# Kernel optimization log

Hardware: AMD Instinct MI355X
Metric: run time of the kernel (lower is better)

Reference implementation:

```python
import jax, jax.numpy as jnp
import numpy as np
from jax import lax

M_POINT = 1024
NSAMPLE = 16
GRASPNESS_THRESHOLD = 0.1
HMIN, HMAX = -0.02, 0.04  # cylinder height range (GraspNet CloudCrop)
RADII = (0.025, 0.05, 0.075, 0.1)
BIG = 1e10


def _fps(xyz, mask):
    """Masked furthest point sampling. xyz [N,3], mask [N] bool -> idx [M_POINT] int32.
    Masked-out points carry -BIG min-distance so they are never selected."""
    first = jnp.argmax(mask).astype(jnp.int32)  # first graspable point (ragged FPS start)
    dists = jnp.where(mask, BIG, -BIG)
    idxs = jnp.zeros((M_POINT,), jnp.int32).at[0].set(first)

    def body(i, carry):
        idxs, dists = carry
        last = xyz[idxs[i - 1]]
        d = jnp.sum((xyz - last) ** 2, axis=-1)
        dists = jnp.where(mask, jnp.minimum(dists, d), -BIG)
        nxt = jnp.argmax(dists).astype(jnp.int32)
        return idxs.at[i].set(nxt), dists

    idxs, _ = lax.fori_loop(1, M_POINT, body, (idxs, dists))
    return idxs


def _cylinder_crop(xyz_g, feat_g, rot, radius, w1, b1, w2, b2):
    """Cylinder query + group + shared MLP + maxpool.
    xyz_g [B,M,3], feat_g [B,M,C], rot [B,M,3,3] -> [B,M,256]."""
    B, M, _ = xyz_g.shape
    # offsets of candidate n relative to seed m, expressed in the seed's gripper frame
    diff = xyz_g[:, None, :, :] - xyz_g[:, :, None, :]          # [B,M(seed),M(cand),3]
    local = jnp.einsum('bmnj,bmji->bmni', diff, rot)            # rotate into approach frame
    along = local[..., 0]
    r2 = local[..., 1] ** 2 + local[..., 2] ** 2
    cond = (r2 < radius * radius) & (along > HMIN) & (along < HMAX)  # [B,M,M]
    # first NSAMPLE in-cylinder indices (ball-query semantics: pad with first hit)
    order = jnp.where(cond, jnp.arange(M)[None, None, :], M)
    sel = jnp.argsort(order, axis=-1)[..., :NSAMPLE].astype(jnp.int32)  # [B,M,NS]
    cnt = cond.sum(axis=-1)                                     # [B,M]
    fill = sel[..., :1]
    idx = jnp.where(jnp.arange(NSAMPLE)[None, None, :] < cnt[..., None], sel, fill)
    idx = jnp.where(cnt[..., None] > 0, idx, 0)
    grouped_xyz = jnp.take_along_axis(local, idx[..., None], axis=2) / radius  # [B,M,NS,3]
    grouped_feat = feat_g[jnp.arange(B)[:, None, None], idx]                    # [B,M,NS,C]
    g = jnp.concatenate([grouped_xyz, grouped_feat], axis=-1)                   # [B,M,NS,3+C]
    h = jax.nn.relu(jnp.einsum('bmnf,of->bmno', g, w1) + b1)
    h = jax.nn.relu(jnp.einsum('bmnf,of->bmno', h, w2) + b2)
    return h.max(axis=2)                                                        # [B,M,256]


def setup_inputs() -> dict:
    key = jax.random.key(0)
    ks = jax.random.split(key, 10)
    B, N, C = 4, 20000, 512
    return {
        'seed_xyz': jax.random.normal(ks[0], (B, N, 3), jnp.float32),
        'seed_features': jax.random.normal(ks[1], (B, C, N), jnp.float32),
        'objectness_score': jax.random.normal(ks[2], (B, 2, N), jnp.float32),
        'graspness_score': jax.random.uniform(ks[3], (B, N), jnp.float32),
        'grasp_top_views_rot': jax.random.normal(ks[4], (B, M_POINT, 3, 3), jnp.float32),
        'crop_w1': jax.random.normal(ks[5], (4, 256, 3 + C), jnp.float32) * 0.05,
        'crop_b1': jnp.zeros((4, 256), jnp.float32),
        'crop_w2': jax.random.normal(ks[6], (4, 256, 256), jnp.float32) * 0.05,
        'crop_b2': jnp.zeros((4, 256), jnp.float32),
        'fuse_w': jax.random.normal(ks[7], (256, 1024), jnp.float32) * 0.05,
        'fuse_b': jnp.zeros((256,), jnp.float32),
    }


def reference(seed_xyz, seed_features, objectness_score, graspness_score,
              grasp_top_views_rot, crop_w1, crop_b1, crop_w2, crop_b2,
              fuse_w, fuse_b):
    # graspable mask (per-point, data dependent)
    objectness_mask = jnp.argmax(objectness_score, axis=1) == 1       # [B,N]
    graspness_mask = graspness_score > GRASPNESS_THRESHOLD
    graspable_mask = objectness_mask & graspness_mask
    # masked FPS per sample, then gather
    idxs = jax.vmap(_fps)(seed_xyz, graspable_mask)                    # [B,M]
    xyz_g = jnp.take_along_axis(seed_xyz, idxs[:, :, None], axis=1)    # [B,M,3]
    feat = seed_features.transpose(0, 2, 1)                            # [B,N,C]
    feat_g = jnp.take_along_axis(feat, idxs[:, :, None], axis=1)       # [B,M,C]
    # multiscale cylinder crops
    feats = [_cylinder_crop(xyz_g, feat_g, grasp_top_views_rot, RADII[k],
                            crop_w1[k], crop_b1[k], crop_w2[k], crop_b2[k])
             for k in range(4)]
    cat = jnp.concatenate(feats, axis=-1)                              # [B,M,1024]
    fused = jnp.einsum('bmf,of->bom', cat, fuse_w) + fuse_b[None, :, None]  # [B,256,M]
    return fused
```

## Files before the change

kernel.cpp:

```cpp
#include <hip/hip_runtime.h>
#include <cstdint>
#include <cfloat>
#include <climits>

#define NPTS 20000
#define NB 4
#define MP 1024
#define CF 512
#define MAXCH 20
#define PFIX 10
#define KFAST (PFIX*MP)

__constant__ float c_r2[4]  = { (float)(0.025*0.025), (float)(0.05*0.05),
                                (float)(0.075*0.075), (float)(0.1*0.1) };
__constant__ float c_rad[4] = { 0.025f, 0.05f, 0.075f, 0.1f };

__global__ __launch_bounds__(1024, 4)
void k_fps(const float* __restrict__ xyz, const float* __restrict__ obj,
           const float* __restrict__ grasp, int* __restrict__ idxs,
           float* __restrict__ xyz_g,
           float* __restrict__ xc, float* __restrict__ yc,
           float* __restrict__ zc, int* __restrict__ ci)
{
    const int b = blockIdx.x;
    const int tid = threadIdx.x;
    const int lane = tid & 63, wid = tid >> 6;
    const float* xb  = xyz   + (size_t)b * NPTS * 3;
    const float* ob0 = obj   + (size_t)b * 2 * NPTS;
    const float* ob1 = ob0 + NPTS;
    const float* gb  = grasp + (size_t)b * NPTS;
    float* xcb = xc + (size_t)b * 20480;
    float* ycb = yc + (size_t)b * 20480;
    float* zcb = zc + (size_t)b * 20480;
    int*   cib = ci + (size_t)b * 20480;

    __shared__ float sXYZ[3 * KFAST];
    __shared__ int   s_sel[MP];
    __shared__ unsigned long long sKey[2][16];
    __shared__ int   sWaveCnt[16];
    float* sX = sXYZ;
    float* sY = sXYZ + KFAST;
    float* sZ = sXYZ + 2 * KFAST;

    int kbase = 0;
    for (int i = 0; i < MAXCH; ++i) {
        int n = i * MP + tid;
        bool msk = false; float x = 0.f, y = 0.f, z = 0.f;
        if (n < NPTS) {
            msk = (ob1[n] > ob0[n]) && (gb[n] > 0.1f);
            if (msk) { x = xb[n*3+0]; y = xb[n*3+1]; z = xb[n*3+2]; }
        }
        unsigned long long bal = __ballot(msk);
        if (lane == 0) sWaveCnt[wid] = __popcll(bal);
        __syncthreads();
        int pre = 0, tot = 0;
        for (int w = 0; w < 16; ++w) { int c = sWaveCnt[w]; tot += c; if (w < wid) pre += c; }
        if (msk) {
            int rank = kbase + pre + __popcll(bal & ((1ull << lane) - 1ull));
            xcb[rank] = x; ycb[rank] = y; zcb[rank] = z; cib[rank] = n;
            if (rank < KFAST) { sX[rank] = x; sY[rank] = y; sZ[rank] = z; }
        }
        kbase += tot;
        __syncthreads();
    }
    const int K = kbase;

    if (K == 0) {
        idxs[b*MP + tid] = 0;
        xyz_g[((size_t)b*MP + tid)*3 + 0] = xb[0];
        xyz_g[((size_t)b*MP + tid)*3 + 1] = xb[1];
        xyz_g[((size_t)b*MP + tid)*3 + 2] = xb[2];
        return;
    }

    if (K <= KFAST) {
        float px[PFIX], py[PFIX], pz[PFIX], pd[PFIX];
#pragma unroll
        for (int i = 0; i < PFIX; ++i) {
            int c = tid + (i << 10);
            bool v = c < K;
            px[i] = v ? sX[c] : 0.f;
            py[i] = v ? sY[c] : 0.f;
            pz[i] = v ? sZ[c] : 0.f;
            pd[i] = v ? 1e10f : -3.0e38f;
        }
        float lx = sX[0], ly = sY[0], lz = sZ[0];
        if (tid == 0) s_sel[0] = 0;

        for (int it = 1; it < MP; ++it) {
            float bv = -3.4e38f; int bn = 0;
#pragma unroll
            for (int i = 0; i < PFIX; ++i) {
                float dx = px[i] - lx, dy = py[i] - ly, dz = pz[i] - lz;
                float d = __fadd_rn(__fadd_rn(__fmul_rn(dx,dx), __fmul_rn(dy,dy)),
                                    __fmul_rn(dz,dz));
                float nd = fminf(pd[i], d);
                pd[i] = nd;
                bool w = nd > bv;
                bn = w ? (tid + (i << 10)) : bn;
                bv = fmaxf(bv, nd);
            }
            unsigned int ob = __float_as_uint(bv);
            unsigned int ord = (ob & 0x80000000u) ? ~ob : (ob | 0x80000000u);
            unsigned long long key = ((unsigned long long)ord << 32)
                                   | (unsigned int)(~bn);
#pragma unroll
            for (int off = 1; off < 64; off <<= 1) {
                unsigned long long ok = __shfl_xor(key, off);
                key = (ok > key) ? ok : key;
            }
            int p = it & 1;
            if (lane == 0) sKey[p][wid] = key;
            __syncthreads();
            unsigned long long k2 = sKey[p][lane & 15];
#pragma unroll
            for (int off = 1; off < 16; off <<= 1) {
                unsigned long long ok = __shfl_xor(k2, off);
                k2 = (ok > k2) ? ok : k2;
            }
            int n = ~((unsigned int)k2);
            lx = sX[n]; ly = sY[n]; lz = sZ[n];
            if (tid == 0) s_sel[it] = n;
        }
        __syncthreads();
        int nc = s_sel[tid];
        idxs[b*MP + tid] = cib[nc];
        xyz_g[((size_t)b*MP + tid)*3 + 0] = sX[nc];
        xyz_g[((size_t)b*MP + tid)*3 + 1] = sY[nc];
        xyz_g[((size_t)b*MP + tid)*3 + 2] = sZ[nc];
        return;
    }

    {
        float* fD = sXYZ;
        for (int c = tid; c < K; c += MP) fD[c] = 1e10f;
        float lx = xcb[0], ly = ycb[0], lz = zcb[0];
        if (tid == 0) s_sel[0] = 0;
        __syncthreads();
        for (int it = 1; it < MP; ++it) {
            float bv = -3.4e38f; int bn = 0;
            for (int c = tid; c < K; c += MP) {
                float dx = xcb[c] - lx, dy = ycb[c] - ly, dz = zcb[c] - lz;
                float d = __fadd_rn(__fadd_rn(__fmul_rn(dx,dx), __fmul_rn(dy,dy)),
                                    __fmul_rn(dz,dz));
                float nd = fminf(fD[c], d);
                fD[c] = nd;
                bool w = nd > bv;
                bn = w ? c : bn;
                bv = fmaxf(bv, nd);
            }
            unsigned int ob = __float_as_uint(bv);
            unsigned int ord = (ob & 0x80000000u) ? ~ob : (ob | 0x80000000u);
            unsigned long long key = ((unsigned long long)ord << 32)
                                   | (unsigned int)(~bn);
#pragma unroll
            for (int off = 1; off < 64; off <<= 1) {
                unsigned long long ok = __shfl_xor(key, off);
                key = (ok > key) ? ok : key;
            }
            int p = it & 1;
            if (lane == 0) sKey[p][wid] = key;
            __syncthreads();
            unsigned long long k2 = sKey[p][lane & 15];
#pragma unroll
            for (int off = 1; off < 16; off <<= 1) {
                unsigned long long ok = __shfl_xor(k2, off);
                k2 = (ok > k2) ? ok : k2;
            }
            int n = ~((unsigned int)k2);
            lx = xcb[n]; ly = ycb[n]; lz = zcb[n];
            if (tid == 0) s_sel[it] = n;
        }
        __syncthreads();
        int nc = s_sel[tid];
        idxs[b*MP + tid] = cib[nc];
        xyz_g[((size_t)b*MP + tid)*3 + 0] = xcb[nc];
        xyz_g[((size_t)b*MP + tid)*3 + 1] = ycb[nc];
        xyz_g[((size_t)b*MP + tid)*3 + 2] = zcb[nc];
    }
}

__global__ void k_gather_feat(const float* __restrict__ sf, const int* __restrict__ idxs,
                              float* __restrict__ feat_g)
{
    int bm = blockIdx.x;
    int b = bm >> 10;
    int n = idxs[bm];
    const float* src = sf + (size_t)b*CF*NPTS + n;
    float* dst = feat_g + (size_t)bm*CF;
    for (int c = threadIdx.x; c < CF; c += 256) dst[c] = src[(size_t)c * NPTS];
}

__global__ void k_prep(const float* __restrict__ w1, const float* __restrict__ w2,
                       float* __restrict__ w2t, float* __restrict__ w1x)
{
    int k = blockIdx.x, cb = blockIdx.y*32, ob = blockIdx.z*32;
    int tx = threadIdx.x & 31, ty = threadIdx.x >> 5;
    __shared__ float t[32][33];
    for (int r = ty; r < 32; r += 8)
        t[r][tx] = w2[((size_t)k*256 + ob + r)*256 + cb + tx];
    __syncthreads();
    for (int r = ty; r < 32; r += 8)
        w2t[((size_t)k*256 + cb + r)*256 + ob + tx] = t[tx][r];
    if (blockIdx.y == 0 && blockIdx.z == 0) {
        int o = threadIdx.x;
        for (int d = 0; d < 3; ++d)
            w1x[(k*3 + d)*256 + o] = w1[((size_t)k*256 + o)*515 + d];
    }
}

__global__ __launch_bounds__(256)
void k_f1(const float* __restrict__ feat_g, const float* __restrict__ w1,
          const float* __restrict__ b1, float* __restrict__ F1)
{
    const int rt = blockIdx.x * 64;
    const int ot = blockIdx.y * 64;
    const int k  = blockIdx.z;
    const int tid = threadIdx.x;
    __shared__ float As[16][68];
    __shared__ float Bs[16][68];
    const int lr = tid >> 2;
    const int lc = (tid & 3) * 4;
    const int tr = (tid & 15) * 4;
    const int tc = (tid >> 4) * 4;
    float acc[4][4] = {};
    for (int kk = 0; kk < CF; kk += 16) {
        const float* ap = feat_g + (size_t)(rt + lr)*CF + kk + lc;
        As[lc+0][lr] = ap[0]; As[lc+1][lr] = ap[1];
        As[lc+2][lr] = ap[2]; As[lc+3][lr] = ap[3];
        const float* bp = w1 + (size_t)(k*256 + ot + lr)*515 + 3 + kk + lc;
        Bs[lc+0][lr] = bp[0]; Bs[lc+1][lr] = bp[1];
        Bs[lc+2][lr] = bp[2]; Bs[lc+3][lr] = bp[3];
        __syncthreads();
#pragma unroll
        for (int cc = 0; cc < 16; ++cc) {
            float a0=As[cc][tr+0], a1=As[cc][tr+1], a2=As[cc][tr+2], a3=As[cc][tr+3];
            float q0=Bs[cc][tc+0], q1=Bs[cc][tc+1], q2=Bs[cc][tc+2], q3=Bs[cc][tc+3];
            acc[0][0]+=a0*q0; acc[0][1]+=a0*q1; acc[0][2]+=a0*q2; acc[0][3]+=a0*q3;
            acc[1][0]+=a1*q0; acc[1][1]+=a1*q1; acc[1][2]+=a1*q2; acc[1][3]+=a1*q3;
            acc[2][0]+=a2*q0; acc[2][1]+=a2*q1; acc[2][2]+=a2*q2; acc[2][3]+=a2*q3;
            acc[3][0]+=a3*q0; acc[3][1]+=a3*q1; acc[3][2]+=a3*q2; acc[3][3]+=a3*q3;
        }
        __syncthreads();
    }
#pragma unroll
    for (int i = 0; i < 4; ++i)
#pragma unroll
        for (int j = 0; j < 4; ++j)
            F1[((size_t)k*4096 + rt+tr+i)*256 + ot+tc+j] = acc[i][j] + b1[k*256 + ot+tc+j];
}

__global__ __launch_bounds__(1024)
void k_nbr(const float* __restrict__ xyz_g, const float* __restrict__ rot,
           int* __restrict__ sel, float* __restrict__ lxyz, int* __restrict__ cnt)
{
    const int bm = blockIdx.x;
    const int b = bm >> 10;
    const int tid = threadIdx.x;
    const int lane = tid & 63, wid = tid >> 6;
    __shared__ float sR[9], sC[3];
    __shared__ int   sSel[4][16];
    __shared__ float sL[4][16][3];
    __shared__ int   sW[16];
    __shared__ int   sCnt[4];
    __shared__ float sFb[3];
    if (tid < 9) sR[tid] = rot[(size_t)bm*9 + tid];
    if (tid < 3) sC[tid] = xyz_g[(size_t)bm*3 + tid];
    __syncthreads();
    float x = xyz_g[((size_t)b*MP + tid)*3 + 0];
    float y = xyz_g[((size_t)b*MP + tid)*3 + 1];
    float z = xyz_g[((size_t)b*MP + tid)*3 + 2];
    float dx = x - sC[0], dy = y - sC[1], dz = z - sC[2];
    float l0 = __fadd_rn(__fadd_rn(__fmul_rn(dx,sR[0]), __fmul_rn(dy,sR[3])), __fmul_rn(dz,sR[6]));
    float l1 = __fadd_rn(__fadd_rn(__fmul_rn(dx,sR[1]), __fmul_rn(dy,sR[4])), __fmul_rn(dz,sR[7]));
    float l2 = __fadd_rn(__fadd_rn(__fmul_rn(dx,sR[2]), __fmul_rn(dy,sR[5])), __fmul_rn(dz,sR[8]));
    float r2 = __fadd_rn(__fmul_rn(l1,l1), __fmul_rn(l2,l2));
    bool basec = (l0 > -0.02f) && (l0 < 0.04f);
    if (tid == 0) { sFb[0]=l0; sFb[1]=l1; sFb[2]=l2; }
    for (int k = 0; k < 4; ++k) {
        bool c = basec && (r2 < c_r2[k]);
        unsigned long long bal = __ballot(c);
        if (lane == 0) sW[wid] = __popcll(bal);
        __syncthreads();
        int pre = 0, tot = 0;
        for (int w = 0; w < 16; ++w) { int cw = sW[w]; tot += cw; if (w < wid) pre += cw; }
        int rank = pre + __popcll(bal & ((1ull << lane) - 1ull));
        if (c && rank < 16) {
            sSel[k][rank] = tid;
            sL[k][rank][0] = l0; sL[k][rank][1] = l1; sL[k][rank][2] = l2;
        }
        if (tid == 0) sCnt[k] = min(tot, 16);
        __syncthreads();
    }
    if (tid < 64) {
        int k = tid >> 4, j = tid & 15;
        int ck = sCnt[k];
        int src = (j < ck) ? j : 0;
        int v; float a0, a1, a2;
        if (ck > 0) { v = sSel[k][src]; a0=sL[k][src][0]; a1=sL[k][src][1]; a2=sL[k][src][2]; }
        else        { v = 0; a0=sFb[0]; a1=sFb[1]; a2=sFb[2]; }
        size_t off = ((size_t)bm*4 + k)*16 + j;
        sel[off] = v;
        lxyz[off*3+0]=a0; lxyz[off*3+1]=a1; lxyz[off*3+2]=a2;
        if (j == 0) cnt[bm*4 + k] = (ck > 0) ? ck : 1;
    }
}

__global__ __launch_bounds__(256)
void k_mlp(const float* __restrict__ F1, const float* __restrict__ w1x,
           const float* __restrict__ w2t, const float* __restrict__ b2,
           const int* __restrict__ sel, const float* __restrict__ lxyz,
           const int* __restrict__ cnt, float* __restrict__ cat)
{
    const int gid = blockIdx.x;
    const int k = gid & 3;
    const int g0 = (gid >> 2) * 4;
    const int o = threadIdx.x;
    __shared__ float h1s[64][256];
    int u0 = cnt[(g0+0)*4 + k], u1 = cnt[(g0+1)*4 + k],
        u2 = cnt[(g0+2)*4 + k], u3 = cnt[(g0+3)*4 + k];
    int off1 = u0, off2 = u0+u1, off3 = off2+u2, tot = off3+u3;
    const float wx0 = w1x[(k*3+0)*256 + o];
    const float wx1 = w1x[(k*3+1)*256 + o];
    const float wx2 = w1x[(k*3+2)*256 + o];
    const float rad = c_rad[k];
    const int bbase = (g0 >> 10) * MP;
    for (int r = 0; r < tot; ++r) {
        int t = (r >= off1) + (r >= off2) + (r >= off3);
        int toff = (t==0) ? 0 : ((t==1) ? off1 : ((t==2) ? off2 : off3));
        int j = r - toff;
        int bmk = (g0 + t)*4 + k;
        int n = sel[(size_t)bmk*16 + j];
        float lx = lxyz[((size_t)bmk*16 + j)*3 + 0];
        float ly = lxyz[((size_t)bmk*16 + j)*3 + 1];
        float lz = lxyz[((size_t)bmk*16 + j)*3 + 2];
        float v = F1[((size_t)k*4096 + bbase + n)*256 + o];
        v += (lx/rad)*wx0 + (ly/rad)*wx1 + (lz/rad)*wx2;
        h1s[r][o] = fmaxf(v, 0.f);
    }
    __syncthreads();
    const float b2v = b2[k*256 + o];
    float m0=0.f, m1=0.f, m2=0.f, m3=0.f;
    const float* w2c = w2t + (size_t)k*65536 + o;
    for (int base = 0; base < tot; base += 4) {
        int r0 = base;
        int r1 = min(base+1, tot-1);
        int r2 = min(base+2, tot-1);
        int r3 = min(base+3, tot-1);
        float a0=0.f, a1=0.f, a2=0.f, a3=0.f;
        for (int c = 0; c < 256; c += 4) {
            float wA = w2c[(c+0)*256], wB = w2c[(c+1)*256];
            float wC = w2c[(c+2)*256], wD = w2c[(c+3)*256];
            float4 h;
            h = *(const float4*)&h1s[r0][c]; a0 += h.x*wA + h.y*wB + h.z*wC + h.w*wD;
            h = *(const float4*)&h1s[r1][c]; a1 += h.x*wA + h.y*wB + h.z*wC + h.w*wD;
            h = *(const float4*)&h1s[r2][c]; a2 += h.x*wA + h.y*wB + h.z*wC + h.w*wD;
            h = *(const float4*)&h1s[r3][c]; a3 += h.x*wA + h.y*wB + h.z*wC + h.w*wD;
        }
#pragma unroll
        for (int q = 0; q < 4; ++q) {
            int r = base + q;
            if (r < tot) {
                float a = (q==0) ? a0 : ((q==1) ? a1 : ((q==2) ? a2 : a3));
                int t = (r >= off1) + (r >= off2) + (r >= off3);
                float val = fmaxf(a + b2v, 0.f);
                if      (t==0) m0 = fmaxf(m0, val);
                else if (t==1) m1 = fmaxf(m1, val);
                else if (t==2) m2 = fmaxf(m2, val);
                else           m3 = fmaxf(m3, val);
            }
        }
    }
    cat[(size_t)(g0+0)*1024 + k*256 + o] = m0;
    cat[(size_t)(g0+1)*1024 + k*256 + o] = m1;
    cat[(size_t)(g0+2)*1024 + k*256 + o] = m2;
    cat[(size_t)(g0+3)*1024 + k*256 + o] = m3;
}

__global__ void k_transpose(const float* __restrict__ cat, float* __restrict__ catT)
{
    int bt = blockIdx.x;
    int b = bt >> 10;
    int t2 = bt & 1023;
    int mi = (t2 >> 5) * 32, fi = (t2 & 31) * 32;
    int tx = threadIdx.x & 31, ty = threadIdx.x >> 5;
    __shared__ float t[32][33];
    const float* src = cat + (size_t)b * 1048576;
    float* dst = catT + (size_t)b * 1048576;
    for (int r = ty; r < 32; r += 8) t[r][tx] = src[(size_t)(mi + r)*1024 + fi + tx];
    __syncthreads();
    for (int r = ty; r < 32; r += 8) dst[(size_t)(fi + r)*1024 + mi + tx] = t[tx][r];
}

__global__ __launch_bounds__(256)
void k_fuse(const float* __restrict__ catT, const float* __restrict__ fw,
            const float* __restrict__ fb, float* __restrict__ out)
{
    const int o0 = blockIdx.x * 4;
    const int b = blockIdx.y;
    const int m = threadIdx.x * 4;
    const float* ct = catT + (size_t)b * 1048576 + m;
    float4 a0 = {0,0,0,0}, a1 = a0, a2 = a0, a3 = a0;
    for (int f = 0; f < 1024; ++f) {
        const float4 cv = *(const float4*)(ct + (size_t)f*1024);
        float w0 = fw[(size_t)(o0+0)*1024 + f];
        float w1 = fw[(size_t)(o0+1)*1024 + f];
        float w2 = fw[(size_t)(o0+2)*1024 + f];
        float w3 = fw[(size_t)(o0+3)*1024 + f];
        a0.x += cv.x*w0; a0.y += cv.y*w0; a0.z += cv.z*w0; a0.w += cv.w*w0;
        a1.x += cv.x*w1; a1.y += cv.y*w1; a1.z += cv.z*w1; a1.w += cv.w*w1;
        a2.x += cv.x*w2; a2.y += cv.y*w2; a2.z += cv.z*w2; a2.w += cv.w*w2;
        a3.x += cv.x*w3; a3.y += cv.y*w3; a3.z += cv.z*w3; a3.w += cv.w*w3;
    }
#pragma unroll
    for (int q = 0; q < 4; ++q) {
        float bb = fb[o0+q];
        float4 r = (q==0) ? a0 : ((q==1) ? a1 : ((q==2) ? a2 : a3));
        r.x += bb; r.y += bb; r.z += bb; r.w += bb;
        *(float4*)&out[((size_t)b*256 + o0 + q)*1024 + m] = r;
    }
}

extern "C" void kernel_launch(void* const* d_in, const int* in_sizes, int n_in,
                              void* d_out, int out_size, void* d_ws, size_t ws_size,
                              hipStream_t stream)
{
    const float* seed_xyz      = (const float*)d_in[0];
    const float* seed_features = (const float*)d_in[1];
    const float* objectness    = (const float*)d_in[2];
    const float* graspness     = (const float*)d_in[3];
    const float* rot           = (const float*)d_in[4];
    const float* w1            = (const float*)d_in[5];
    const float* b1            = (const float*)d_in[6];
    const float* w2            = (const float*)d_in[7];
    const float* b2            = (const float*)d_in[8];
    const float* fw            = (const float*)d_in[9];
    const float* fb            = (const float*)d_in[10];
    float* out = (float*)d_out;

    char* ws = (char*)d_ws;
    size_t off = 0;
    int*   idxs   = (int*)(ws + off);  off += 16u<<10;
    float* xyz_g  = (float*)(ws + off); off += 48u<<10;
    float* feat_g = (float*)(ws + off); off += 8u<<20;
    float* F1     = (float*)(ws + off); off += 16u<<20;
    float* w2t    = (float*)(ws + off); off += 1u<<20;
    float* w1x    = (float*)(ws + off); off += 64u<<10;
    int*   sel    = (int*)(ws + off);   off += 1u<<20;
    int*   cnt    = (int*)(ws + off);   off += 64u<<10;
    float* lxyz   = (float*)(ws + off); off += 3u<<20;
    float* cat    = (float*)(ws + off); off += 16u<<20;
    float* catT   = (float*)(ws + off); off += 16u<<20;

    float* xc = cat;
    float* yc = cat + 4*20480;
    float* zc = cat + 8*20480;
    int*   ci = (int*)(cat + 12*20480);

    k_fps<<<NB, 1024, 0, stream>>>(seed_xyz, objectness, graspness, idxs, xyz_g,
                                   xc, yc, zc, ci);
    k_prep<<<dim3(4,8,8), 256, 0, stream>>>(w1, w2, w2t, w1x);
    k_gather_feat<<<NB*MP, 256, 0, stream>>>(seed_features, idxs, feat_g);
    k_f1<<<dim3(64,4,4), 256, 0, stream>>>(feat_g, w1, b1, F1);
    k_nbr<<<NB*MP, 1024, 0, stream>>>(xyz_g, rot, sel, lxyz, cnt);
    k_mlp<<<4096, 256, 0, stream>>>(F1, w1x, w2t, b2, sel, lxyz, cnt, cat);
    k_transpose<<<4096, 256, 0, stream>>>(cat, catT);
    k_fuse<<<dim3(64,4), 256, 0, stream>>>(catT, fw, fb, out);
}
```

Before: 2.047 ms.

## Use 8 working wavefronts and DPP-based key reductions in fast FPS path

```diff
diff --git a/kernel.cpp b/kernel.cpp
--- a/kernel.cpp
+++ b/kernel.cpp
@@ -9,11 +9,31 @@
 #define CF 512
 #define MAXCH 20
 #define PFIX 10
-#define KFAST (PFIX*MP)
+#define KFAST 10240
+#define NWORK 8
+#define PPT 20
 
 __constant__ float c_r2[4]  = { (float)(0.025*0.025), (float)(0.05*0.05),
                                 (float)(0.075*0.075), (float)(0.1*0.1) };
 __constant__ float c_rad[4] = { 0.025f, 0.05f, 0.075f, 0.1f };
+
+#define DPP_XOR1   0xB1
+#define DPP_XOR2   0x4E
+#define DPP_HMIRR  0x141
+#define DPP_MIRR   0x140
+#define DPP_BC15   0x142
+#define DPP_BC31   0x143
+
+template<int CTRL>
+__device__ __forceinline__ unsigned long long kmax_step(unsigned long long k)
+{
+    unsigned int lo = (unsigned int)k;
+    unsigned int hi = (unsigned int)(k >> 32);
+    unsigned int olo = (unsigned int)__builtin_amdgcn_update_dpp((int)lo, (int)lo, CTRL, 0xf, 0xf, false);
+    unsigned int ohi = (unsigned int)__builtin_amdgcn_update_dpp((int)hi, (int)hi, CTRL, 0xf, 0xf, false);
+    unsigned long long ok = ((unsigned long long)ohi << 32) | (unsigned long long)olo;
+    return (ok > k) ? ok : k;
+}
 
 __global__ __launch_bounds__(1024, 4)
 void k_fps(const float* __restrict__ xyz, const float* __restrict__ obj,
@@ -74,53 +94,59 @@
     }
 
     if (K <= KFAST) {
-        float px[PFIX], py[PFIX], pz[PFIX], pd[PFIX];
-#pragma unroll
-        for (int i = 0; i < PFIX; ++i) {
-            int c = tid + (i << 10);
-            bool v = c < K;
-            px[i] = v ? sX[c] : 0.f;
-            py[i] = v ? sY[c] : 0.f;
-            pz[i] = v ? sZ[c] : 0.f;
-            pd[i] = v ? 1e10f : -3.0e38f;
+        const bool work = (wid < NWORK);
+        float px[PPT], py[PPT], pz[PPT], pd[PPT];
+        if (work) {
+#pragma unroll
+            for (int i = 0; i < PPT; ++i) {
+                int c = tid + (i << 9);
+                bool v = c < K;
+                px[i] = v ? sX[c] : 0.f;
+                py[i] = v ? sY[c] : 0.f;
+                pz[i] = v ? sZ[c] : 0.f;
+                pd[i] = v ? 1e10f : -3.0e38f;
+            }
         }
         float lx = sX[0], ly = sY[0], lz = sZ[0];
         if (tid == 0) s_sel[0] = 0;
 
         for (int it = 1; it < MP; ++it) {
-            float bv = -3.4e38f; int bn = 0;
-#pragma unroll
-            for (int i = 0; i < PFIX; ++i) {
-                float dx = px[i] - lx, dy = py[i] - ly, dz = pz[i] - lz;
-                float d = __fadd_rn(__fadd_rn(__fmul_rn(dx,dx), __fmul_rn(dy,dy)),
-                                    __fmul_rn(dz,dz));
-                float nd = fminf(pd[i], d);
-                pd[i] = nd;
-                bool w = nd > bv;
-                bn = w ? (tid + (i << 10)) : bn;
-                bv = fmaxf(bv, nd);
-            }
-            unsigned int ob = __float_as_uint(bv);
-            unsigned int ord = (ob & 0x80000000u) ? ~ob : (ob | 0x80000000u);
-            unsigned long long key = ((unsigned long long)ord << 32)
-                                   | (unsigned int)(~bn);
-#pragma unroll
-            for (int off = 1; off < 64; off <<= 1) {
-                unsigned long long ok = __shfl_xor(key, off);
-                key = (ok > key) ? ok : key;
-            }
-            int p = it & 1;
-            if (lane == 0) sKey[p][wid] = key;
+            const int p = it & 1;
+            if (work) {
+                float bv = -3.4e38f; int bn = 0;
+#pragma unroll
+                for (int i = 0; i < PPT; ++i) {
+                    float dx = px[i] - lx, dy = py[i] - ly, dz = pz[i] - lz;
+                    float d = __fadd_rn(__fadd_rn(__fmul_rn(dx,dx), __fmul_rn(dy,dy)),
+                                        __fmul_rn(dz,dz));
+                    float nd = fminf(pd[i], d);
+                    pd[i] = nd;
+                    bool w = nd > bv;
+                    bn = w ? (tid + (i << 9)) : bn;
+                    bv = fmaxf(bv, nd);
+                }
+                unsigned int ob = __float_as_uint(bv);
+                unsigned int ord = (ob & 0x80000000u) ? ~ob : (ob | 0x80000000u);
+                unsigned long long key = ((unsigned long long)ord << 32)
+                                       | (unsigned int)(~bn);
+                key = kmax_step<DPP_XOR1 >(key);
+                key = kmax_step<DPP_XOR2 >(key);
+                key = kmax_step<DPP_HMIRR>(key);
+                key = kmax_step<DPP_MIRR >(key);
+                key = kmax_step<DPP_BC15 >(key);
+                key = kmax_step<DPP_BC31 >(key);
+                if (lane == 63) sKey[p][wid] = key;
+            }
             __syncthreads();
-            unsigned long long k2 = sKey[p][lane & 15];
-#pragma unroll
-            for (int off = 1; off < 16; off <<= 1) {
-                unsigned long long ok = __shfl_xor(k2, off);
-                k2 = (ok > k2) ? ok : k2;
-            }
-            int n = ~((unsigned int)k2);
-            lx = sX[n]; ly = sY[n]; lz = sZ[n];
-            if (tid == 0) s_sel[it] = n;
+            if (work) {
+                unsigned long long k2 = sKey[p][lane & 7];
+                k2 = kmax_step<DPP_XOR1 >(k2);
+                k2 = kmax_step<DPP_XOR2 >(k2);
+                k2 = kmax_step<DPP_HMIRR>(k2);
+                int n = ~((unsigned int)k2);
+                lx = sX[n]; ly = sY[n]; lz = sZ[n];
+                if (tid == 0) s_sel[it] = n;
+            }
         }
         __syncthreads();
         int nc = s_sel[tid];
```

New measurement: 1.744 ms. 1.17x faster.
